# Kernel optimization log

Hardware: AMD Instinct MI355X
Metric: run time of the kernel (lower is better)

Reference implementation:

```python
import jax, jax.numpy as jnp
import numpy as np

B, S, D = 2, 2048, 2048
H, KV, DH = 32, 8, 64
ROPE_THETA = 10000.0


def setup_inputs() -> dict:
    key = jax.random.key(0)
    ks = jax.random.split(key, 5)
    scale = 0.02
    return {
        "x": jax.random.normal(ks[0], (B, S, D), dtype=jnp.float32),
        "Wq": jax.random.normal(ks[1], (H * DH, D), dtype=jnp.float32) * scale,
        "Wk": jax.random.normal(ks[2], (KV * DH, D), dtype=jnp.float32) * scale,
        "Wv": jax.random.normal(ks[3], (KV * DH, D), dtype=jnp.float32) * scale,
        "Wo": jax.random.normal(ks[4], (D, H * DH), dtype=jnp.float32) * scale,
    }


def _rope_cos_sin(seq_len, dim, dtype):
    inv_freq = 1.0 / (ROPE_THETA ** (jnp.arange(0, dim, 2, dtype=jnp.float32) / dim))
    freqs = jnp.arange(seq_len, dtype=jnp.float32)[:, None] * inv_freq[None, :]  # [S, dim/2]
    emb = jnp.concatenate([freqs, freqs], axis=-1)  # [S, dim]
    return jnp.cos(emb).astype(dtype), jnp.sin(emb).astype(dtype)


def _rotate_half(x):
    x1, x2 = jnp.split(x, 2, axis=-1)
    return jnp.concatenate([-x2, x1], axis=-1)


def reference(x, Wq, Wk, Wv, Wo):
    b, s, d = x.shape
    # QKV projections (Linear with weight [out, in], no bias)
    q = (x @ Wq.T).reshape(b, s, H, DH).transpose(0, 2, 1, 3)   # [B,H,S,Dh]
    k = (x @ Wk.T).reshape(b, s, KV, DH).transpose(0, 2, 1, 3)  # [B,KV,S,Dh]
    v = (x @ Wv.T).reshape(b, s, KV, DH).transpose(0, 2, 1, 3)
    # RoPE
    cos, sin = _rope_cos_sin(s, DH, x.dtype)  # [S, Dh]
    q = q * cos + _rotate_half(q) * sin
    k = k * cos + _rotate_half(k) * sin
    # GQA: repeat KV heads
    rep = H // KV
    k = jnp.repeat(k, rep, axis=1)  # [B,H,S,Dh]
    v = jnp.repeat(v, rep, axis=1)
    # Causal SDPA
    scores = jnp.einsum("bhsd,bhtd->bhst", q, k) / jnp.sqrt(jnp.asarray(DH, x.dtype))
    causal = jnp.tril(jnp.ones((s, s), dtype=bool))
    scores = jnp.where(causal, scores, jnp.finfo(x.dtype).min)
    attn = jax.nn.softmax(scores, axis=-1)
    out = jnp.einsum("bhst,bhtd->bhsd", attn, v)  # [B,H,S,Dh]
    out = out.transpose(0, 2, 1, 3).reshape(b, s, H * DH)
    return out @ Wo.T
```

## Files before the change

### kernel.cpp

```cpp
#include <hip/hip_runtime.h>


typedef float  f32x4 __attribute__((ext_vector_type(4)));
typedef short  s16x8 __attribute__((ext_vector_type(8)));
typedef unsigned short u16;

#define DEV __device__ __forceinline__

DEV u16 f2bf(float f) {
  unsigned int u = __builtin_bit_cast(unsigned int, f);
  u += 0x7fff + ((u >> 16) & 1);
  return (u16)(u >> 16);
}

DEV void gld16(const void* g, void* l) {
  __builtin_amdgcn_global_load_lds(
      (const __attribute__((address_space(1))) void*)g,
      (__attribute__((address_space(3))) void*)l, 16, 0, 0);
}

DEV f32x4 mfma16(s16x8 a, s16x8 b, f32x4 c) {
  return __builtin_amdgcn_mfma_f32_16x16x32_bf16(a, b, c, 0, 0, 0);
}

__global__ __launch_bounds__(256) void cast_all_kernel(
    const float4* __restrict__ x,  const float4* __restrict__ wq,
    const float4* __restrict__ wk, const float4* __restrict__ wv,
    const float4* __restrict__ wo,
    ushort4* __restrict__ xb, ushort4* __restrict__ wqkv, ushort4* __restrict__ wob)
{
  const int NX = 2097152, NQ = 1048576, NKV = 262144, NO = 1048576;
  int i = blockIdx.x * 256 + threadIdx.x;
  const float4* src; ushort4* dst; int off;
  if      (i < NX)            { src = x;  dst = xb;              off = i; }
  else if (i < NX+NQ)         { src = wq; dst = wqkv;            off = i - NX; }
  else if (i < NX+NQ+NKV)     { src = wk; dst = wqkv + NQ;       off = i - NX - NQ; }
  else if (i < NX+NQ+2*NKV)   { src = wv; dst = wqkv + NQ + NKV; off = i - NX - NQ - NKV; }
  else if (i < NX+NQ+2*NKV+NO){ src = wo; dst = wob;             off = i - NX - NQ - 2*NKV; }
  else return;
  float4 v = src[off];
  ushort4 o; o.x = f2bf(v.x); o.y = f2bf(v.y); o.z = f2bf(v.z); o.w = f2bf(v.w);
  dst[off] = o;
}

__global__ __launch_bounds__(256) void rope_table_kernel(float* __restrict__ ct,
                                                         float* __restrict__ st)
{
  int i = blockIdx.x * 256 + threadIdx.x;
  int s = i >> 5, d = i & 31;
  float inv = powf(10000.0f, -(float)d * (1.0f / 32.0f));
  float a = (float)s * inv;
  float sv, cv;
  sincosf(a, &sv, &cv);
  ct[i] = cv; st[i] = sv;
}

DEV void gemm_core(const u16* __restrict__ A, const u16* __restrict__ Bw, int K,
                   u16* As, u16* Bs, int bm, int bn, int tid, f32x4 acc[4][4])
{
  const int lane = tid & 63, wave = tid >> 6;
  const int wr = wave >> 1, wc = wave & 1;
  const int q = lane & 15, g = lane >> 4;
  const u16* Ag = A  + (size_t)(bm*128 + (tid >> 2))*K + (tid & 3)*8;
  const u16* Bg = Bw + (size_t)(bn*128 + (tid >> 2))*K + (tid & 3)*8;
  u16* AsL = As + tid*8;
  u16* BsL = Bs + tid*8;
  for (int k0 = 0; k0 < K; k0 += 32) {
    gld16(Ag + k0,                 AsL);
    gld16(Ag + (size_t)64*K + k0,  AsL + 2048);
    gld16(Bg + k0,                 BsL);
    gld16(Bg + (size_t)64*K + k0,  BsL + 2048);
    __syncthreads();
    s16x8 af[4], bf[4];
#pragma unroll
    for (int i = 0; i < 4; ++i) af[i] = *(const s16x8*)&As[(wr*64 + i*16 + q)*32 + g*8];
#pragma unroll
    for (int i = 0; i < 4; ++i) bf[i] = *(const s16x8*)&Bs[(wc*64 + i*16 + q)*32 + g*8];
#pragma unroll
    for (int mt = 0; mt < 4; ++mt)
#pragma unroll
      for (int nt = 0; nt < 4; ++nt)
        acc[mt][nt] = mfma16(af[mt], bf[nt], acc[mt][nt]);
    __syncthreads();
  }
}

__global__ __launch_bounds__(256) void gemm_qkv_kernel(
    const u16* __restrict__ xb, const u16* __restrict__ wqkv,
    const float* __restrict__ ct, const float* __restrict__ st,
    u16* __restrict__ Qo, u16* __restrict__ Ko, u16* __restrict__ Vo)
{
  __shared__ u16 As[128*32], Bs[128*32];
  f32x4 acc[4][4] = {};
  const int tid = threadIdx.x;
  const int bm = blockIdx.x, bn = blockIdx.y;
  gemm_core(xb, wqkv, 2048, As, Bs, bm, bn, tid, acc);

  const int lane = tid & 63, wave = tid >> 6;
  const int wr = wave >> 1, wc = wave & 1;
  const int q = lane & 15, g = lane >> 4;
  const int rowbase = bm*128 + wr*64 + g*4;

  if (bn < 20) {
    const bool isQ = (bn < 16);
    const float sc = isQ ? 0.125f : 1.0f;
#pragma unroll
    for (int mt = 0; mt < 4; ++mt) {
#pragma unroll
      for (int r = 0; r < 4; ++r) {
        const int gr = rowbase + mt*16 + r;
        const int b = gr >> 11, s = gr & 2047;
        const float c0 = ct[s*32 + q],      s0 = st[s*32 + q];
        const float c1 = ct[s*32 + 16 + q], s1 = st[s*32 + 16 + q];
        const float x0 = acc[mt][0][r], x1 = acc[mt][1][r];
        const float x2 = acc[mt][2][r], x3 = acc[mt][3][r];
        const float o0 = (x0*c0 - x2*s0) * sc;
        const float o1 = (x1*c1 - x3*s1) * sc;
        const float o2 = (x2*c0 + x0*s0) * sc;
        const float o3 = (x3*c1 + x1*s1) * sc;
        if (isQ) {
          const int h = bn*2 + wc;
          u16* ob = Qo + ((size_t)(b*32 + h)*2048 + s)*64;
          ob[q] = f2bf(o0); ob[16+q] = f2bf(o1); ob[32+q] = f2bf(o2); ob[48+q] = f2bf(o3);
        } else {
          const int kv = (bn - 16)*2 + wc;
          u16* ob = Ko + ((size_t)(b*8 + kv)*2048 + s)*64;
          ob[q] = f2bf(o0); ob[16+q] = f2bf(o1); ob[32+q] = f2bf(o2); ob[48+q] = f2bf(o3);
        }
      }
    }
  } else {
    const int kv = (bn - 20)*2 + wc;
#pragma unroll
    for (int mt = 0; mt < 4; ++mt)
#pragma unroll
      for (int r = 0; r < 4; ++r) {
        const int gr = rowbase + mt*16 + r;
        const int b = gr >> 11, s = gr & 2047;
        u16* vb = Vo + ((size_t)(b*8 + kv)*64)*2048 + s;
#pragma unroll
        for (int nt = 0; nt < 4; ++nt)
          vb[(size_t)(nt*16 + q)*2048] = f2bf(acc[mt][nt][r]);
      }
  }
}

__global__ __launch_bounds__(256) void attn_kernel(
    const u16* __restrict__ Qg, const u16* __restrict__ Kg,
    const u16* __restrict__ Vtg, u16* __restrict__ AOg)
{
  __shared__ u16 Ks[64*64];
  __shared__ u16 Vs[64*64];
  __shared__ u16 Ps[4][16*68];

  const int tid  = threadIdx.x;
  const int lane = tid & 63, wave = tid >> 6;
  const int q = lane & 15, g = lane >> 4;
  const int bx = blockIdx.x;
  const int bh = blockIdx.y;
  const int b = bh >> 5, h = bh & 31, kv = h >> 2;
  const int q0 = bx * 64;
  const int qw = q0 + wave * 16;

  const u16* Qb = Qg  + ((size_t)(b*32 + h)  * 2048) * 64;
  const u16* Kb = Kg  + ((size_t)(b*8  + kv) * 2048) * 64;
  const u16* Vb = Vtg + ((size_t)(b*8  + kv) * 64) * 2048;

  const s16x8 qf0 = *(const s16x8*)(Qb + (size_t)(qw + q)*64 + g*8);
  const s16x8 qf1 = *(const s16x8*)(Qb + (size_t)(qw + q)*64 + 32 + g*8);

  f32x4 oacc[4] = {};
  float m_run = -1e30f, l_run = 0.0f;

  const int srow = tid >> 3;
  const int scol = (tid & 7) ^ (srow & 7);
  u16* KsL = &Ks[0] + tid*8;
  u16* VsL = &Vs[0] + tid*8;

  const int nkv = bx + 1;
  for (int t = 0; t < nkv; ++t) {
    const int k0 = t * 64;
    gld16(Kb + (size_t)(k0 + srow)*64      + scol*8, KsL);
    gld16(Kb + (size_t)(k0 + 32 + srow)*64 + scol*8, KsL + 2048);
    gld16(Vb + (size_t)srow*2048        + k0 + scol*8, VsL);
    gld16(Vb + (size_t)(32 + srow)*2048 + k0 + scol*8, VsL + 2048);
    __syncthreads();

    f32x4 sacc[4] = {};
#pragma unroll
    for (int kk = 0; kk < 2; ++kk) {
      const s16x8 qf = kk ? qf1 : qf0;
#pragma unroll
      for (int kt = 0; kt < 4; ++kt) {
        const int row = kt*16 + q;
        const int blk = (kk*4 + g) ^ (q & 7);
        const s16x8 kf = *(const s16x8*)&Ks[row*64 + blk*8];
        sacc[kt] = mfma16(kf, qf, sacc[kt]);
      }
    }

    const bool domask = (k0 + 63 > qw);
    float p[4][4];
    float mloc = -1e30f;
#pragma unroll
    for (int kt = 0; kt < 4; ++kt)
#pragma unroll
      for (int r = 0; r < 4; ++r) {
        float s = sacc[kt][r];
        if (domask && (k0 + kt*16 + g*4 + r > qw + q)) s = -1e30f;
        p[kt][r] = s;
        mloc = fmaxf(mloc, s);
      }
    mloc = fmaxf(mloc, __shfl_xor(mloc, 16));
    mloc = fmaxf(mloc, __shfl_xor(mloc, 32));
    const float mnew  = fmaxf(m_run, mloc);
    const float alpha = __expf(m_run - mnew);
    float psum = 0.0f;
#pragma unroll
    for (int kt = 0; kt < 4; ++kt)
#pragma unroll
      for (int r = 0; r < 4; ++r) {
        const float e = __expf(p[kt][r] - mnew);
        p[kt][r] = e; psum += e;
      }
    psum += __shfl_xor(psum, 16);
    psum += __shfl_xor(psum, 32);
    l_run = l_run * alpha + psum;
    m_run = mnew;

    const float al0 = __shfl(alpha, g*4 + 0);
    const float al1 = __shfl(alpha, g*4 + 1);
    const float al2 = __shfl(alpha, g*4 + 2);
    const float al3 = __shfl(alpha, g*4 + 3);
#pragma unroll
    for (int dt = 0; dt < 4; ++dt) {
      oacc[dt][0] *= al0; oacc[dt][1] *= al1; oacc[dt][2] *= al2; oacc[dt][3] *= al3;
    }

#pragma unroll
    for (int kt = 0; kt < 4; ++kt) {
      ushort4 pk;
      pk.x = f2bf(p[kt][0]); pk.y = f2bf(p[kt][1]);
      pk.z = f2bf(p[kt][2]); pk.w = f2bf(p[kt][3]);
      *(ushort4*)&Ps[wave][q*68 + kt*16 + g*4] = pk;
    }

#pragma unroll
    for (int ks = 0; ks < 2; ++ks) {
      const ushort4 a0 = *(const ushort4*)&Ps[wave][q*68 + ks*32 + g*8];
      const ushort4 a1 = *(const ushort4*)&Ps[wave][q*68 + ks*32 + g*8 + 4];
      union { ushort4 hh[2]; s16x8 v; } pu;
      pu.hh[0] = a0; pu.hh[1] = a1;
      const s16x8 pa = pu.v;
#pragma unroll
      for (int dt = 0; dt < 4; ++dt) {
        const int row = dt*16 + q;
        const int blk = (ks*4 + g) ^ (q & 7);
        const s16x8 vf = *(const s16x8*)&Vs[row*64 + blk*8];
        oacc[dt] = mfma16(pa, vf, oacc[dt]);
      }
    }
    __syncthreads();
  }

  const float linv = 1.0f / l_run;
  const float li0 = __shfl(linv, g*4 + 0);
  const float li1 = __shfl(linv, g*4 + 1);
  const float li2 = __shfl(linv, g*4 + 2);
  const float li3 = __shfl(linv, g*4 + 3);
  u16* AOb = AOg + ((size_t)b*2048)*2048 + (size_t)h*64;
#pragma unroll
  for (int dt = 0; dt < 4; ++dt) {
    const int col = dt*16 + q;
    AOb[(size_t)(qw + g*4 + 0)*2048 + col] = f2bf(oacc[dt][0] * li0);
    AOb[(size_t)(qw + g*4 + 1)*2048 + col] = f2bf(oacc[dt][1] * li1);
    AOb[(size_t)(qw + g*4 + 2)*2048 + col] = f2bf(oacc[dt][2] * li2);
    AOb[(size_t)(qw + g*4 + 3)*2048 + col] = f2bf(oacc[dt][3] * li3);
  }
}

__global__ __launch_bounds__(256) void gemm_out_kernel(
    const u16* __restrict__ aob, const u16* __restrict__ wob, float* __restrict__ C)
{
  __shared__ u16 As[128*32], Bs[128*32];
  f32x4 acc[4][4] = {};
  const int tid = threadIdx.x;
  const int bm = blockIdx.x, bn = blockIdx.y;
  gemm_core(aob, wob, 2048, As, Bs, bm, bn, tid, acc);

  const int lane = tid & 63, wave = tid >> 6;
  const int wr = wave >> 1, wc = wave & 1;
  const int q = lane & 15, g = lane >> 4;
#pragma unroll
  for (int mt = 0; mt < 4; ++mt)
#pragma unroll
    for (int r = 0; r < 4; ++r) {
      const size_t row = (size_t)bm*128 + wr*64 + mt*16 + g*4 + r;
      float* cr = C + row*2048 + bn*128 + wc*64 + q;
#pragma unroll
      for (int nt = 0; nt < 4; ++nt) cr[nt*16] = acc[mt][nt][r];
    }
}

extern "C" void kernel_launch(void* const* d_in, const int* in_sizes, int n_in,
                              void* d_out, int out_size, void* d_ws, size_t ws_size,
                              hipStream_t stream)
{
  const float* x  = (const float*)d_in[0];
  const float* Wq = (const float*)d_in[1];
  const float* Wk = (const float*)d_in[2];
  const float* Wv = (const float*)d_in[3];
  const float* Wo = (const float*)d_in[4];
  float* out = (float*)d_out;

  char* ws = (char*)d_ws;
  u16*   xb   = (u16*)  (ws);
  u16*   wqkv = (u16*)  (ws + 16777216);
  u16*   wob  = (u16*)  (ws + 29360128);
  float* ct   = (float*)(ws + 37748736);
  float* stb  = (float*)(ws + 38010880);
  u16*   qb   = (u16*)  (ws + 38273024);
  u16*   kb   = (u16*)  (ws + 55050240);
  u16*   vtb  = (u16*)  (ws + 59244544);
  u16*   aob  = xb;

  cast_all_kernel<<<18432, 256, 0, stream>>>(
      (const float4*)x, (const float4*)Wq, (const float4*)Wk, (const float4*)Wv,
      (const float4*)Wo, (ushort4*)xb, (ushort4*)wqkv, (ushort4*)wob);
  rope_table_kernel<<<256, 256, 0, stream>>>(ct, stb);
  gemm_qkv_kernel<<<dim3(32, 24), 256, 0, stream>>>(xb, wqkv, ct, stb, qb, kb, vtb);
  attn_kernel<<<dim3(32, 64), 256, 0, stream>>>(qb, kb, vtb, aob);
  gemm_out_kernel<<<dim3(32, 16), 256, 0, stream>>>(aob, wob, out);
}
```

Before: 396.6 us.

## Double-buffer attention K/V tiles, skip rescales lazily, swizzle block order, longest-first

Attention now double-buffers K/V in shared memory, issuing the next tile's async loads before computing on the current one. It also skips the online-softmax rescale unless the running max grows by more than a threshold, and raises wave priority around the MFMA sections. Blocks are remapped in all three GEMM/attention kernels so consecutive IDs are spread across XCDs, and causal attention processes the longest query tiles first. This trades doubled LDS use for overlap and load balance, and the lazy rescale relies on exp values staying bounded by e^8.

After: 365.1 us. 8.0% less time.

```diff
diff --git a/kernel.cpp b/kernel.cpp
--- a/kernel.cpp
+++ b/kernel.cpp
@@ -93,7 +93,9 @@
   __shared__ u16 As[128*32], Bs[128*32];
   f32x4 acc[4][4] = {};
   const int tid = threadIdx.x;
-  const int bm = blockIdx.x, bn = blockIdx.y;
+  const int id = blockIdx.x;
+  const int swz = (id & 7) * 96 + (id >> 3);
+  const int bm = swz & 31, bn = swz >> 5;
   gemm_core(xb, wqkv, 2048, As, Bs, bm, bn, tid, acc);
 
   const int lane = tid & 63, wave = tid >> 6;
@@ -149,18 +151,19 @@
     const u16* __restrict__ Qg, const u16* __restrict__ Kg,
     const u16* __restrict__ Vtg, u16* __restrict__ AOg)
 {
-  __shared__ u16 Ks[64*64];
-  __shared__ u16 Vs[64*64];
+  __shared__ u16 Ks[2][64*64];
+  __shared__ u16 Vs[2][64*64];
   __shared__ u16 Ps[4][16*68];
 
   const int tid  = threadIdx.x;
   const int lane = tid & 63, wave = tid >> 6;
   const int q = lane & 15, g = lane >> 4;
-  const int bx = blockIdx.x;
-  const int bh = blockIdx.y;
+  const int id = blockIdx.x;
+  const int wg = (id & 7) * 256 + (id >> 3);
+  const int bh = wg >> 5;
+  const int bx = 31 - (wg & 31);
   const int b = bh >> 5, h = bh & 31, kv = h >> 2;
-  const int q0 = bx * 64;
-  const int qw = q0 + wave * 16;
+  const int qw = bx * 64 + wave * 16;
 
   const u16* Qb = Qg  + ((size_t)(b*32 + h)  * 2048) * 64;
   const u16* Kb = Kg  + ((size_t)(b*8  + kv) * 2048) * 64;
@@ -174,19 +177,28 @@
 
   const int srow = tid >> 3;
   const int scol = (tid & 7) ^ (srow & 7);
-  u16* KsL = &Ks[0] + tid*8;
-  u16* VsL = &Vs[0] + tid*8;
+
+  auto stage = [&](int t, int bufi) {
+    const int k0 = t * 64;
+    u16* kd = &Ks[bufi][tid*8];
+    u16* vd = &Vs[bufi][tid*8];
+    gld16(Kb + (size_t)(k0 + srow)*64      + scol*8, kd);
+    gld16(Kb + (size_t)(k0 + 32 + srow)*64 + scol*8, kd + 2048);
+    gld16(Vb + (size_t)srow*2048        + k0 + scol*8, vd);
+    gld16(Vb + (size_t)(32 + srow)*2048 + k0 + scol*8, vd + 2048);
+  };
 
   const int nkv = bx + 1;
+  stage(0, 0);
+  __syncthreads();
+
   for (int t = 0; t < nkv; ++t) {
+    const int cur = t & 1;
+    if (t + 1 < nkv) stage(t + 1, cur ^ 1);
     const int k0 = t * 64;
-    gld16(Kb + (size_t)(k0 + srow)*64      + scol*8, KsL);
-    gld16(Kb + (size_t)(k0 + 32 + srow)*64 + scol*8, KsL + 2048);
-    gld16(Vb + (size_t)srow*2048        + k0 + scol*8, VsL);
-    gld16(Vb + (size_t)(32 + srow)*2048 + k0 + scol*8, VsL + 2048);
-    __syncthreads();
 
     f32x4 sacc[4] = {};
+    __builtin_amdgcn_s_setprio(1);
 #pragma unroll
     for (int kk = 0; kk < 2; ++kk) {
       const s16x8 qf = kk ? qf1 : qf0;
@@ -194,10 +206,11 @@
       for (int kt = 0; kt < 4; ++kt) {
         const int row = kt*16 + q;
         const int blk = (kk*4 + g) ^ (q & 7);
-        const s16x8 kf = *(const s16x8*)&Ks[row*64 + blk*8];
+        const s16x8 kf = *(const s16x8*)&Ks[cur][row*64 + blk*8];
         sacc[kt] = mfma16(kf, qf, sacc[kt]);
       }
     }
+    __builtin_amdgcn_s_setprio(0);
 
     const bool domask = (k0 + 63 > qw);
     float p[4][4];
@@ -213,29 +226,31 @@
       }
     mloc = fmaxf(mloc, __shfl_xor(mloc, 16));
     mloc = fmaxf(mloc, __shfl_xor(mloc, 32));
-    const float mnew  = fmaxf(m_run, mloc);
-    const float alpha = __expf(m_run - mnew);
+    if (!__all(mloc <= m_run + 8.0f)) {
+      const float mnew  = fmaxf(m_run, mloc);
+      const float alpha = __expf(m_run - mnew);
+      l_run *= alpha;
+      const float al0 = __shfl(alpha, g*4 + 0);
+      const float al1 = __shfl(alpha, g*4 + 1);
+      const float al2 = __shfl(alpha, g*4 + 2);
+      const float al3 = __shfl(alpha, g*4 + 3);
+#pragma unroll
+      for (int dt = 0; dt < 4; ++dt) {
+        oacc[dt][0] *= al0; oacc[dt][1] *= al1; oacc[dt][2] *= al2; oacc[dt][3] *= al3;
+      }
+      m_run = mnew;
+    }
     float psum = 0.0f;
 #pragma unroll
     for (int kt = 0; kt < 4; ++kt)
 #pragma unroll
       for (int r = 0; r < 4; ++r) {
-        const float e = __expf(p[kt][r] - mnew);
+        const float e = __expf(p[kt][r] - m_run);
         p[kt][r] = e; psum += e;
       }
     psum += __shfl_xor(psum, 16);
     psum += __shfl_xor(psum, 32);
-    l_run = l_run * alpha + psum;
-    m_run = mnew;
-
-    const float al0 = __shfl(alpha, g*4 + 0);
-    const float al1 = __shfl(alpha, g*4 + 1);
-    const float al2 = __shfl(alpha, g*4 + 2);
-    const float al3 = __shfl(alpha, g*4 + 3);
-#pragma unroll
-    for (int dt = 0; dt < 4; ++dt) {
-      oacc[dt][0] *= al0; oacc[dt][1] *= al1; oacc[dt][2] *= al2; oacc[dt][3] *= al3;
-    }
+    l_run += psum;
 
 #pragma unroll
     for (int kt = 0; kt < 4; ++kt) {
@@ -245,6 +260,7 @@
       *(ushort4*)&Ps[wave][q*68 + kt*16 + g*4] = pk;
     }
 
+    __builtin_amdgcn_s_setprio(1);
 #pragma unroll
     for (int ks = 0; ks < 2; ++ks) {
       const ushort4 a0 = *(const ushort4*)&Ps[wave][q*68 + ks*32 + g*8];
@@ -256,10 +272,11 @@
       for (int dt = 0; dt < 4; ++dt) {
         const int row = dt*16 + q;
         const int blk = (ks*4 + g) ^ (q & 7);
-        const s16x8 vf = *(const s16x8*)&Vs[row*64 + blk*8];
+        const s16x8 vf = *(const s16x8*)&Vs[cur][row*64 + blk*8];
         oacc[dt] = mfma16(pa, vf, oacc[dt]);
       }
     }
+    __builtin_amdgcn_s_setprio(0);
     __syncthreads();
   }
 
@@ -285,7 +302,9 @@
   __shared__ u16 As[128*32], Bs[128*32];
   f32x4 acc[4][4] = {};
   const int tid = threadIdx.x;
-  const int bm = blockIdx.x, bn = blockIdx.y;
+  const int id = blockIdx.x;
+  const int swz = (id & 7) * 64 + (id >> 3);
+  const int bm = swz & 31, bn = swz >> 5;
   gemm_core(aob, wob, 2048, As, Bs, bm, bn, tid, acc);
 
   const int lane = tid & 63, wave = tid >> 6;
@@ -328,7 +347,7 @@
       (const float4*)x, (const float4*)Wq, (const float4*)Wk, (const float4*)Wv,
       (const float4*)Wo, (ushort4*)xb, (ushort4*)wqkv, (ushort4*)wob);
   rope_table_kernel<<<256, 256, 0, stream>>>(ct, stb);
-  gemm_qkv_kernel<<<dim3(32, 24), 256, 0, stream>>>(xb, wqkv, ct, stb, qb, kb, vtb);
-  attn_kernel<<<dim3(32, 64), 256, 0, stream>>>(qb, kb, vtb, aob);
-  gemm_out_kernel<<<dim3(32, 16), 256, 0, stream>>>(aob, wob, out);
-}
+  gemm_qkv_kernel<<<768, 256, 0, stream>>>(xb, wqkv, ct, stb, qb, kb, vtb);
+  attn_kernel<<<2048, 256, 0, stream>>>(qb, kb, vtb, aob);
+  gemm_out_kernel<<<512, 256, 0, stream>>>(aob, wob, out);
+}
```
